# Kernel optimization log

Hardware: AMD Instinct MI355X
Metric: run time of the kernel (lower is better)

Reference implementation:

```python
import jax, jax.numpy as jnp
import numpy as np

N = 5000      # batch entities / prompts
M = 50000     # flattened neighbors
R = 500000    # flattened (neighbor, relation) pairs
D = 768
VOCAB = 10000


def setup_inputs() -> dict:
    key = jax.random.key(0)
    ks = jax.random.split(key, 12)
    start_emb = jax.random.normal(ks[0], (N, D), dtype=jnp.float32)
    prompt_emb = jax.random.normal(ks[1], (N, D), dtype=jnp.float32)
    relation_emb = jax.random.normal(ks[2], (R, D), dtype=jnp.float32)
    neighbor_emb = jax.random.normal(ks[3], (M, D), dtype=jnp.float32)
    count_table = jax.random.normal(ks[4], (VOCAB, D), dtype=jnp.float32) * 0.02
    W = jax.random.normal(ks[5], (1, 4 * D), dtype=jnp.float32) * 0.02
    b = jnp.zeros((1,), dtype=jnp.float32)
    counts = jax.random.randint(ks[6], (R,), 0, VOCAB)
    rel_start_idx = jax.random.randint(ks[7], (R,), 0, N)
    neighbor_idx = jnp.sort(jax.random.randint(ks[8], (R,), 0, M))
    start_idx = jax.random.randint(ks[9], (M,), 0, N)
    return {
        "start_emb": start_emb, "prompt_emb": prompt_emb,
        "relation_emb": relation_emb, "neighbor_emb": neighbor_emb,
        "count_table": count_table, "W": W, "b": b,
        "counts": counts, "rel_start_idx": rel_start_idx,
        "neighbor_idx": neighbor_idx, "start_idx": start_idx,
    }


def _segment_softmax(logits, seg, num_segments):
    # numerically stable softmax within each neighbor segment
    seg_max = jax.ops.segment_max(logits, seg, num_segments=num_segments)
    ex = jnp.exp(logits - seg_max[seg])
    denom = jax.ops.segment_sum(ex, seg, num_segments=num_segments)
    return ex / denom[seg]


def reference(start_emb, prompt_emb, relation_emb, neighbor_emb,
              count_table, W, b,
              counts, rel_start_idx, neighbor_idx, start_idx):
    num_neighbors = neighbor_emb.shape[0]
    # relation_emb = relation_emb * count_embs(counts)   [R, D]
    rel = relation_emb * count_table[counts]
    # per-relation logit: <start_emb[rel_start_idx], rel>  [R]
    s_rel = start_emb[rel_start_idx]
    logits = jnp.sum(s_rel * rel, axis=1)
    # scatter_softmax over neighbor segments, then scatter_add aggregation
    alpha = _segment_softmax(logits, neighbor_idx, num_neighbors)
    rel_agg = jax.ops.segment_sum(rel * alpha[:, None], neighbor_idx,
                                  num_segments=num_neighbors)  # [M, D]
    # gather per-neighbor start / prompt embeddings
    s_n = start_emb[start_idx]      # [M, D]
    p_n = prompt_emb[start_idx]     # [M, D]
    # AttentionScorer: concat then Linear(4D -> 1), squeeze
    combined = jnp.concatenate([s_n, p_n, rel_agg, neighbor_emb], axis=1)
    score = (combined @ W.T + b).squeeze(-1)  # [M]
    return score
```

## Files before the change

### kernel.cpp

```cpp
#include <hip/hip_runtime.h>
#include <math.h>

#define WAVE 64

__device__ inline float wave_reduce_sum(float v) {
    #pragma unroll
    for (int off = 32; off > 0; off >>= 1)
        v += __shfl_xor(v, off, WAVE);
    return v;
}

__device__ inline unsigned int f32_to_e4m3(float a) {
    unsigned int u = __float_as_uint(a);
    unsigned int sgn = (u >> 31) << 7;
    unsigned int absu = u & 0x7FFFFFFFu;
    if (absu < 0x3C800000u) return sgn;
    int exp = (int)(absu >> 23) - 127;
    unsigned int m = absu & 0x7FFFFFu;
    unsigned int keep = m >> 20;
    unsigned int rest = m & 0xFFFFFu;
    if (rest > 0x80000u || (rest == 0x80000u && (keep & 1u))) keep++;
    if (keep == 8u) { keep = 0u; exp += 1; }
    if (exp > 8) { exp = 8; keep = 7u; }
    return sgn | ((unsigned int)(exp + 7) << 3) | keep;
}

__device__ inline float e4m3_to_f32(unsigned int b) {
    unsigned int expm = b & 0x7Fu;
    unsigned int f = ((b & 0x80u) << 24) | ((expm + (120u << 3)) << 20);
    float v = __uint_as_float(f);
    return (expm & 0x78u) ? v : 0.0f;
}

__device__ inline void decode4_fp8(unsigned int u, float& a, float& b, float& c, float& d) {
#if __has_builtin(__builtin_amdgcn_cvt_pk_f32_fp8)
    auto lo = __builtin_amdgcn_cvt_pk_f32_fp8(u, false);
    auto hi = __builtin_amdgcn_cvt_pk_f32_fp8(u, true);
    a = lo[0]; b = lo[1]; c = hi[0]; d = hi[1];
#else
    a = e4m3_to_f32(u & 0xFFu);
    b = e4m3_to_f32((u >> 8) & 0xFFu);
    c = e4m3_to_f32((u >> 16) & 0xFFu);
    d = e4m3_to_f32((u >> 24) & 0xFFu);
#endif
}

__global__ void cvt_fp8_kernel(const float* __restrict__ in,
                               unsigned int* __restrict__ out,
                               int n4, float scale) {
    int i = blockIdx.x * blockDim.x + threadIdx.x;
    if (i >= n4) return;
    float4 v = ((const float4*)in)[i];
    unsigned int b0 = f32_to_e4m3(v.x * scale);
    unsigned int b1 = f32_to_e4m3(v.y * scale);
    unsigned int b2 = f32_to_e4m3(v.z * scale);
    unsigned int b3 = f32_to_e4m3(v.w * scale);
    out[i] = b0 | (b1 << 8) | (b2 << 16) | (b3 << 24);
}

__global__ void entity_dots_kernel(const float* __restrict__ start_emb,
                                   const float* __restrict__ prompt_emb,
                                   const float* __restrict__ W,
                                   float* __restrict__ ew, int N, int D) {
    int wavesPerBlock = blockDim.x >> 6;
    int i = blockIdx.x * wavesPerBlock + (threadIdx.x >> 6);
    int lane = threadIdx.x & 63;
    if (i >= N) return;
    const float* s  = start_emb  + (size_t)i * D;
    const float* p  = prompt_emb + (size_t)i * D;
    const float* w0 = W;
    const float* w1 = W + D;
    float acc = 0.f;
    for (int idx = lane * 4; idx < D; idx += WAVE * 4) {
        float4 sv  = *(const float4*)(s  + idx);
        float4 pv  = *(const float4*)(p  + idx);
        float4 w0v = *(const float4*)(w0 + idx);
        float4 w1v = *(const float4*)(w1 + idx);
        acc = fmaf(sv.x, w0v.x, acc);
        acc = fmaf(sv.y, w0v.y, acc);
        acc = fmaf(sv.z, w0v.z, acc);
        acc = fmaf(sv.w, w0v.w, acc);
        acc = fmaf(pv.x, w1v.x, acc);
        acc = fmaf(pv.y, w1v.y, acc);
        acc = fmaf(pv.z, w1v.z, acc);
        acc = fmaf(pv.w, w1v.w, acc);
    }
    acc = wave_reduce_sum(acc);
    if (lane == 0) ew[i] = acc;
}

__global__ void relation_kernel(const float* __restrict__ relation_emb,
                                const unsigned char* __restrict__ ctf8,
                                const unsigned char* __restrict__ sf8,
                                const float* __restrict__ W,
                                const int* __restrict__ counts,
                                const int* __restrict__ rel_start_idx,
                                float2* __restrict__ lt,
                                int R, int D, float inv_ct_scale) {
    int wavesPerBlock = blockDim.x >> 6;
    int r = blockIdx.x * wavesPerBlock + (threadIdx.x >> 6);
    int lane = threadIdx.x & 63;
    if (r >= R) return;
    const float* re = relation_emb + (size_t)r * D;
    const unsigned int* ct = (const unsigned int*)(ctf8 + (size_t)counts[r] * D);
    const unsigned int* se = (const unsigned int*)(sf8 + (size_t)rel_start_idx[r] * D);
    const float* w2 = W + 2 * (size_t)D;
    float lg = 0.f, tt = 0.f;
    for (int idx = lane * 4; idx < D; idx += WAVE * 4) {
        float4 rv = *(const float4*)(re + idx);
        float4 wv = *(const float4*)(w2 + idx);
        unsigned int cu = ct[idx >> 2];
        unsigned int su = se[idx >> 2];
        float c0, c1, c2, c3, s0, s1, s2, s3;
        decode4_fp8(cu, c0, c1, c2, c3);
        decode4_fp8(su, s0, s1, s2, s3);
        float relx = rv.x * c0;
        float rely = rv.y * c1;
        float relz = rv.z * c2;
        float relw = rv.w * c3;
        lg = fmaf(s0, relx, lg);
        lg = fmaf(s1, rely, lg);
        lg = fmaf(s2, relz, lg);
        lg = fmaf(s3, relw, lg);
        tt = fmaf(wv.x, relx, tt);
        tt = fmaf(wv.y, rely, tt);
        tt = fmaf(wv.z, relz, tt);
        tt = fmaf(wv.w, relw, tt);
    }
    lg = wave_reduce_sum(lg) * inv_ct_scale;
    tt = wave_reduce_sum(tt) * inv_ct_scale;
    if (lane == 0) lt[r] = make_float2(lg, tt);
}

__global__ void segment_kernel(const float2* __restrict__ lt,
                               const int* __restrict__ neighbor_idx,
                               float* __restrict__ c,
                               int M, int R) {
    int m = blockIdx.x * blockDim.x + threadIdx.x;
    if (m >= M) return;
    int lo = 0, hi = R;
    while (lo < hi) {
        int mid = (lo + hi) >> 1;
        if (neighbor_idx[mid] < m) lo = mid + 1; else hi = mid;
    }
    int s = lo;
    hi = R;
    while (lo < hi) {
        int mid = (lo + hi) >> 1;
        if (neighbor_idx[mid] < m + 1) lo = mid + 1; else hi = mid;
    }
    int e = lo;
    if (e <= s) { c[m] = 0.f; return; }
    float mx = -INFINITY;
    for (int i = s; i < e; ++i) mx = fmaxf(mx, lt[i].x);
    float den = 0.f, num = 0.f;
    for (int i = s; i < e; ++i) {
        float2 v = lt[i];
        float ex = expf(v.x - mx);
        den += ex;
        num = fmaf(ex, v.y, num);
    }
    c[m] = num / den;
}

__global__ void score_kernel(const float* __restrict__ neighbor_emb,
                             const float* __restrict__ W,
                             const float* __restrict__ bptr,
                             const int* __restrict__ start_idx,
                             const float* __restrict__ ew,
                             const float* __restrict__ c,
                             float* __restrict__ out,
                             int M, int D) {
    int wavesPerBlock = blockDim.x >> 6;
    int m = blockIdx.x * wavesPerBlock + (threadIdx.x >> 6);
    int lane = threadIdx.x & 63;
    if (m >= M) return;
    const float* nb = neighbor_emb + (size_t)m * D;
    const float* w3 = W + 3 * (size_t)D;
    float acc = 0.f;
    for (int idx = lane * 4; idx < D; idx += WAVE * 4) {
        float4 nv = *(const float4*)(nb + idx);
        float4 wv = *(const float4*)(w3 + idx);
        acc = fmaf(nv.x, wv.x, acc);
        acc = fmaf(nv.y, wv.y, acc);
        acc = fmaf(nv.z, wv.z, acc);
        acc = fmaf(nv.w, wv.w, acc);
    }
    acc = wave_reduce_sum(acc);
    if (lane == 0) {
        out[m] = acc + ew[start_idx[m]] + c[m] + bptr[0];
    }
}

extern "C" void kernel_launch(void* const* d_in, const int* in_sizes, int n_in,
                              void* d_out, int out_size, void* d_ws, size_t ws_size,
                              hipStream_t stream) {
    const float* start_emb    = (const float*)d_in[0];
    const float* prompt_emb   = (const float*)d_in[1];
    const float* relation_emb = (const float*)d_in[2];
    const float* neighbor_emb = (const float*)d_in[3];
    const float* count_table  = (const float*)d_in[4];
    const float* W            = (const float*)d_in[5];
    const float* b            = (const float*)d_in[6];
    const int*   counts        = (const int*)d_in[7];
    const int*   rel_start_idx = (const int*)d_in[8];
    const int*   neighbor_idx  = (const int*)d_in[9];
    const int*   start_idx     = (const int*)d_in[10];

    int D = in_sizes[5] / 4;
    int N = in_sizes[0] / D;
    int R = in_sizes[7];
    int M = in_sizes[10];
    int VOCAB = in_sizes[4] / D;

    const float CT_SCALE = 64.0f;

    char* ws = (char*)d_ws;
    size_t off = 0;
    float*  ew   = (float*)(ws + off);  off += ((size_t)N * 4 + 255) & ~(size_t)255;
    float2* lt   = (float2*)(ws + off); off += ((size_t)R * 8 + 255) & ~(size_t)255;
    float*  c    = (float*)(ws + off);  off += ((size_t)M * 4 + 255) & ~(size_t)255;
    unsigned char* ctf8 = (unsigned char*)(ws + off); off += ((size_t)VOCAB * D + 255) & ~(size_t)255;
    unsigned char* sf8  = (unsigned char*)(ws + off); off += ((size_t)N * D + 255) & ~(size_t)255;
    float*  out  = (float*)d_out;

    {
        int n4 = (VOCAB * D) / 4;
        cvt_fp8_kernel<<<(n4 + 255) / 256, 256, 0, stream>>>(count_table,
                                                             (unsigned int*)ctf8, n4, CT_SCALE);
        int m4 = (N * D) / 4;
        cvt_fp8_kernel<<<(m4 + 255) / 256, 256, 0, stream>>>(start_emb,
                                                             (unsigned int*)sf8, m4, 1.0f);
    }
    {
        int grid = (N + 3) / 4;
        entity_dots_kernel<<<grid, 256, 0, stream>>>(start_emb, prompt_emb, W, ew, N, D);
    }
    {
        int grid = (R + 3) / 4;
        relation_kernel<<<grid, 256, 0, stream>>>(relation_emb, ctf8, sf8, W,
                                                  counts, rel_start_idx, lt, R, D,
                                                  1.0f / CT_SCALE);
    }
    {
        int grid = (M + 255) / 256;
        segment_kernel<<<grid, 256, 0, stream>>>(lt, neighbor_idx, c, M, R);
    }
    {
        int grid = (M + 3) / 4;
        score_kernel<<<grid, 256, 0, stream>>>(neighbor_emb, W, b, start_idx, ew, c, out, M, D);
    }
}
```

Measured before the change: 375.4 us.

## Fuse prologue kernels, merge segment softmax into score, persist relation waves

Merges the two fp8 conversion kernels and the entity-dot kernel into one prologue launch. The segment softmax moves into the score kernel and is now computed cooperatively by a wave instead of a single thread, which removes one launch and the intermediate c buffer. The relation and score kernels get D=768 specialised variants that use a persistent grid, keep W slices in registers, prefetch the next indices, and use nontemporal loads for streamed rows. In exchange, every wave in the score kernel now runs the two binary searches redundantly, and the fixed 2048-block grid may not fill the device optimally.

```diff
diff --git a/kernel.cpp b/kernel.cpp
--- a/kernel.cpp
+++ b/kernel.cpp
@@ -2,11 +2,19 @@
 #include <math.h>
 
 #define WAVE 64
+
+typedef float f32x4 __attribute__((ext_vector_type(4)));
 
 __device__ inline float wave_reduce_sum(float v) {
     #pragma unroll
     for (int off = 32; off > 0; off >>= 1)
         v += __shfl_xor(v, off, WAVE);
+    return v;
+}
+__device__ inline float wave_reduce_max(float v) {
+    #pragma unroll
+    for (int off = 32; off > 0; off >>= 1)
+        v = fmaxf(v, __shfl_xor(v, off, WAVE));
     return v;
 }
 
@@ -45,25 +53,49 @@
 #endif
 }
 
-__global__ void cvt_fp8_kernel(const float* __restrict__ in,
-                               unsigned int* __restrict__ out,
-                               int n4, float scale) {
-    int i = blockIdx.x * blockDim.x + threadIdx.x;
-    if (i >= n4) return;
-    float4 v = ((const float4*)in)[i];
-    unsigned int b0 = f32_to_e4m3(v.x * scale);
-    unsigned int b1 = f32_to_e4m3(v.y * scale);
-    unsigned int b2 = f32_to_e4m3(v.z * scale);
-    unsigned int b3 = f32_to_e4m3(v.w * scale);
-    out[i] = b0 | (b1 << 8) | (b2 << 16) | (b3 << 24);
-}
-
-__global__ void entity_dots_kernel(const float* __restrict__ start_emb,
-                                   const float* __restrict__ prompt_emb,
-                                   const float* __restrict__ W,
-                                   float* __restrict__ ew, int N, int D) {
-    int wavesPerBlock = blockDim.x >> 6;
-    int i = blockIdx.x * wavesPerBlock + (threadIdx.x >> 6);
+__device__ inline unsigned int pack4_fp8(float4 v, float scale) {
+    return f32_to_e4m3(v.x * scale) | (f32_to_e4m3(v.y * scale) << 8) |
+           (f32_to_e4m3(v.z * scale) << 16) | (f32_to_e4m3(v.w * scale) << 24);
+}
+
+__global__ __launch_bounds__(256) void prologue_kernel(
+        const float* __restrict__ count_table,
+        const float* __restrict__ start_emb,
+        const float* __restrict__ prompt_emb,
+        const float* __restrict__ W,
+        unsigned int* __restrict__ ctf8,
+        unsigned int* __restrict__ sf8,
+        float* __restrict__ ew,
+        int ctN16, int sN16, int B_ct, int B_s,
+        int N, int D, float ct_scale) {
+    int b = blockIdx.x;
+    if (b < B_ct) {
+        int i = b * 256 + threadIdx.x;
+        if (i < ctN16) {
+            const float4* in = (const float4*)count_table + (size_t)i * 4;
+            uint4 o;
+            o.x = pack4_fp8(in[0], ct_scale);
+            o.y = pack4_fp8(in[1], ct_scale);
+            o.z = pack4_fp8(in[2], ct_scale);
+            o.w = pack4_fp8(in[3], ct_scale);
+            ((uint4*)ctf8)[i] = o;
+        }
+        return;
+    }
+    if (b < B_ct + B_s) {
+        int i = (b - B_ct) * 256 + threadIdx.x;
+        if (i < sN16) {
+            const float4* in = (const float4*)start_emb + (size_t)i * 4;
+            uint4 o;
+            o.x = pack4_fp8(in[0], 1.0f);
+            o.y = pack4_fp8(in[1], 1.0f);
+            o.z = pack4_fp8(in[2], 1.0f);
+            o.w = pack4_fp8(in[3], 1.0f);
+            ((uint4*)sf8)[i] = o;
+        }
+        return;
+    }
+    int i = (b - B_ct - B_s) * 4 + (threadIdx.x >> 6);
     int lane = threadIdx.x & 63;
     if (i >= N) return;
     const float* s  = start_emb  + (size_t)i * D;
@@ -89,16 +121,147 @@
     if (lane == 0) ew[i] = acc;
 }
 
-__global__ void relation_kernel(const float* __restrict__ relation_emb,
-                                const unsigned char* __restrict__ ctf8,
-                                const unsigned char* __restrict__ sf8,
-                                const float* __restrict__ W,
-                                const int* __restrict__ counts,
-                                const int* __restrict__ rel_start_idx,
-                                float2* __restrict__ lt,
-                                int R, int D, float inv_ct_scale) {
-    int wavesPerBlock = blockDim.x >> 6;
-    int r = blockIdx.x * wavesPerBlock + (threadIdx.x >> 6);
+__global__ __launch_bounds__(256) void relation_kernel768(
+        const float* __restrict__ relation_emb,
+        const unsigned char* __restrict__ ctf8,
+        const unsigned char* __restrict__ sf8,
+        const float* __restrict__ W,
+        const int* __restrict__ counts,
+        const int* __restrict__ rel_start_idx,
+        float2* __restrict__ lt,
+        int R, float inv_ct_scale) {
+    const int D = 768;
+    int lane = threadIdx.x & 63;
+    int gwave = (blockIdx.x * blockDim.x + threadIdx.x) >> 6;
+    int nwaves = (gridDim.x * blockDim.x) >> 6;
+    if (gwave >= R) return;
+
+    const float* w2 = W + 2 * D;
+    float4 wv0 = *(const float4*)(w2 + lane * 4);
+    float4 wv1 = *(const float4*)(w2 + lane * 4 + 256);
+    float4 wv2 = *(const float4*)(w2 + lane * 4 + 512);
+
+    int r = gwave;
+    int cnt = counts[r], st = rel_start_idx[r];
+    while (r < R) {
+        int rn = r + nwaves;
+        int cnt_cur = cnt, st_cur = st;
+        if (rn < R) { cnt = counts[rn]; st = rel_start_idx[rn]; }
+
+        const float* re = relation_emb + (size_t)r * D;
+        const unsigned int* ct = (const unsigned int*)(ctf8 + (size_t)cnt_cur * D);
+        const unsigned int* se = (const unsigned int*)(sf8 + (size_t)st_cur * D);
+
+        f32x4 a0 = __builtin_nontemporal_load((const f32x4*)(re + lane * 4));
+        f32x4 a1 = __builtin_nontemporal_load((const f32x4*)(re + lane * 4 + 256));
+        f32x4 a2 = __builtin_nontemporal_load((const f32x4*)(re + lane * 4 + 512));
+        unsigned int cu0 = ct[lane], cu1 = ct[lane + 64], cu2 = ct[lane + 128];
+        unsigned int su0 = se[lane], su1 = se[lane + 64], su2 = se[lane + 128];
+
+        float lg = 0.f, tt = 0.f;
+        {
+            float c0,c1,c2,c3, s0,s1,s2,s3;
+            decode4_fp8(cu0, c0,c1,c2,c3);
+            decode4_fp8(su0, s0,s1,s2,s3);
+            float x0 = a0.x*c0, x1 = a0.y*c1, x2 = a0.z*c2, x3 = a0.w*c3;
+            lg = fmaf(s0,x0, fmaf(s1,x1, fmaf(s2,x2, fmaf(s3,x3, lg))));
+            tt = fmaf(wv0.x,x0, fmaf(wv0.y,x1, fmaf(wv0.z,x2, fmaf(wv0.w,x3, tt))));
+        }
+        {
+            float c0,c1,c2,c3, s0,s1,s2,s3;
+            decode4_fp8(cu1, c0,c1,c2,c3);
+            decode4_fp8(su1, s0,s1,s2,s3);
+            float x0 = a1.x*c0, x1 = a1.y*c1, x2 = a1.z*c2, x3 = a1.w*c3;
+            lg = fmaf(s0,x0, fmaf(s1,x1, fmaf(s2,x2, fmaf(s3,x3, lg))));
+            tt = fmaf(wv1.x,x0, fmaf(wv1.y,x1, fmaf(wv1.z,x2, fmaf(wv1.w,x3, tt))));
+        }
+        {
+            float c0,c1,c2,c3, s0,s1,s2,s3;
+            decode4_fp8(cu2, c0,c1,c2,c3);
+            decode4_fp8(su2, s0,s1,s2,s3);
+            float x0 = a2.x*c0, x1 = a2.y*c1, x2 = a2.z*c2, x3 = a2.w*c3;
+            lg = fmaf(s0,x0, fmaf(s1,x1, fmaf(s2,x2, fmaf(s3,x3, lg))));
+            tt = fmaf(wv2.x,x0, fmaf(wv2.y,x1, fmaf(wv2.z,x2, fmaf(wv2.w,x3, tt))));
+        }
+        lg = wave_reduce_sum(lg) * inv_ct_scale;
+        tt = wave_reduce_sum(tt) * inv_ct_scale;
+        if (lane == 0) lt[r] = make_float2(lg, tt);
+        r = rn;
+    }
+}
+
+__global__ __launch_bounds__(256) void score_kernel768(
+        const float* __restrict__ neighbor_emb,
+        const float* __restrict__ W,
+        const float* __restrict__ bptr,
+        const int* __restrict__ start_idx,
+        const float* __restrict__ ew,
+        const float2* __restrict__ lt,
+        const int* __restrict__ neighbor_idx,
+        float* __restrict__ out,
+        int M, int R) {
+    const int D = 768;
+    int lane = threadIdx.x & 63;
+    int gwave = (blockIdx.x * blockDim.x + threadIdx.x) >> 6;
+    int nwaves = (gridDim.x * blockDim.x) >> 6;
+    const float* w3 = W + 3 * D;
+    float4 wv0 = *(const float4*)(w3 + lane * 4);
+    float4 wv1 = *(const float4*)(w3 + lane * 4 + 256);
+    float4 wv2 = *(const float4*)(w3 + lane * 4 + 512);
+    float bb = bptr[0];
+
+    for (int m = gwave; m < M; m += nwaves) {
+        int lo = 0, hi = R;
+        while (lo < hi) { int mid = (lo + hi) >> 1; if (neighbor_idx[mid] < m) lo = mid + 1; else hi = mid; }
+        int s = lo;
+        hi = R;
+        while (lo < hi) { int mid = (lo + hi) >> 1; if (neighbor_idx[mid] < m + 1) lo = mid + 1; else hi = mid; }
+        int e = lo;
+
+        const float* nb = neighbor_emb + (size_t)m * D;
+        f32x4 a0 = __builtin_nontemporal_load((const f32x4*)(nb + lane * 4));
+        f32x4 a1 = __builtin_nontemporal_load((const f32x4*)(nb + lane * 4 + 256));
+        f32x4 a2 = __builtin_nontemporal_load((const f32x4*)(nb + lane * 4 + 512));
+
+        float cval = 0.f;
+        if (e > s) {
+            float mx = -INFINITY;
+            for (int i = s + lane; i < e; i += WAVE) mx = fmaxf(mx, lt[i].x);
+            mx = wave_reduce_max(mx);
+            float den = 0.f, num = 0.f;
+            for (int i = s + lane; i < e; i += WAVE) {
+                float2 v = lt[i];
+                float exv = expf(v.x - mx);
+                den += exv;
+                num = fmaf(exv, v.y, num);
+            }
+            den = wave_reduce_sum(den);
+            num = wave_reduce_sum(num);
+            cval = num / den;
+        }
+
+        float acc = 0.f;
+        acc = fmaf(a0.x, wv0.x, acc); acc = fmaf(a0.y, wv0.y, acc);
+        acc = fmaf(a0.z, wv0.z, acc); acc = fmaf(a0.w, wv0.w, acc);
+        acc = fmaf(a1.x, wv1.x, acc); acc = fmaf(a1.y, wv1.y, acc);
+        acc = fmaf(a1.z, wv1.z, acc); acc = fmaf(a1.w, wv1.w, acc);
+        acc = fmaf(a2.x, wv2.x, acc); acc = fmaf(a2.y, wv2.y, acc);
+        acc = fmaf(a2.z, wv2.z, acc); acc = fmaf(a2.w, wv2.w, acc);
+        acc = wave_reduce_sum(acc);
+
+        if (lane == 0) out[m] = acc + ew[start_idx[m]] + cval + bb;
+    }
+}
+
+__global__ void relation_kernel_gen(const float* __restrict__ relation_emb,
+                                    const unsigned char* __restrict__ ctf8,
+                                    const unsigned char* __restrict__ sf8,
+                                    const float* __restrict__ W,
+                                    const int* __restrict__ counts,
+                                    const int* __restrict__ rel_start_idx,
+                                    float2* __restrict__ lt,
+                                    int R, int D, float inv_ct_scale) {
+    int r = blockIdx.x * (blockDim.x >> 6) + (threadIdx.x >> 6);
     int lane = threadIdx.x & 63;
     if (r >= R) return;
     const float* re = relation_emb + (size_t)r * D;
@@ -109,72 +272,52 @@
     for (int idx = lane * 4; idx < D; idx += WAVE * 4) {
         float4 rv = *(const float4*)(re + idx);
         float4 wv = *(const float4*)(w2 + idx);
-        unsigned int cu = ct[idx >> 2];
-        unsigned int su = se[idx >> 2];
-        float c0, c1, c2, c3, s0, s1, s2, s3;
-        decode4_fp8(cu, c0, c1, c2, c3);
-        decode4_fp8(su, s0, s1, s2, s3);
-        float relx = rv.x * c0;
-        float rely = rv.y * c1;
-        float relz = rv.z * c2;
-        float relw = rv.w * c3;
-        lg = fmaf(s0, relx, lg);
-        lg = fmaf(s1, rely, lg);
-        lg = fmaf(s2, relz, lg);
-        lg = fmaf(s3, relw, lg);
-        tt = fmaf(wv.x, relx, tt);
-        tt = fmaf(wv.y, rely, tt);
-        tt = fmaf(wv.z, relz, tt);
-        tt = fmaf(wv.w, relw, tt);
+        float c0,c1,c2,c3, s0,s1,s2,s3;
+        decode4_fp8(ct[idx >> 2], c0,c1,c2,c3);
+        decode4_fp8(se[idx >> 2], s0,s1,s2,s3);
+        float x0 = rv.x*c0, x1 = rv.y*c1, x2 = rv.z*c2, x3 = rv.w*c3;
+        lg = fmaf(s0,x0, fmaf(s1,x1, fmaf(s2,x2, fmaf(s3,x3, lg))));
+        tt = fmaf(wv.x,x0, fmaf(wv.y,x1, fmaf(wv.z,x2, fmaf(wv.w,x3, tt))));
     }
     lg = wave_reduce_sum(lg) * inv_ct_scale;
     tt = wave_reduce_sum(tt) * inv_ct_scale;
     if (lane == 0) lt[r] = make_float2(lg, tt);
 }
 
-__global__ void segment_kernel(const float2* __restrict__ lt,
-                               const int* __restrict__ neighbor_idx,
-                               float* __restrict__ c,
-                               int M, int R) {
-    int m = blockIdx.x * blockDim.x + threadIdx.x;
+__global__ void score_kernel_gen(const float* __restrict__ neighbor_emb,
+                                 const float* __restrict__ W,
+                                 const float* __restrict__ bptr,
+                                 const int* __restrict__ start_idx,
+                                 const float* __restrict__ ew,
+                                 const float2* __restrict__ lt,
+                                 const int* __restrict__ neighbor_idx,
+                                 float* __restrict__ out,
+                                 int M, int R, int D) {
+    int m = blockIdx.x * (blockDim.x >> 6) + (threadIdx.x >> 6);
+    int lane = threadIdx.x & 63;
     if (m >= M) return;
     int lo = 0, hi = R;
-    while (lo < hi) {
-        int mid = (lo + hi) >> 1;
-        if (neighbor_idx[mid] < m) lo = mid + 1; else hi = mid;
-    }
+    while (lo < hi) { int mid = (lo + hi) >> 1; if (neighbor_idx[mid] < m) lo = mid + 1; else hi = mid; }
     int s = lo;
     hi = R;
-    while (lo < hi) {
-        int mid = (lo + hi) >> 1;
-        if (neighbor_idx[mid] < m + 1) lo = mid + 1; else hi = mid;
-    }
+    while (lo < hi) { int mid = (lo + hi) >> 1; if (neighbor_idx[mid] < m + 1) lo = mid + 1; else hi = mid; }
     int e = lo;
-    if (e <= s) { c[m] = 0.f; return; }
-    float mx = -INFINITY;
-    for (int i = s; i < e; ++i) mx = fmaxf(mx, lt[i].x);
-    float den = 0.f, num = 0.f;
-    for (int i = s; i < e; ++i) {
-        float2 v = lt[i];
-        float ex = expf(v.x - mx);
-        den += ex;
-        num = fmaf(ex, v.y, num);
-    }
-    c[m] = num / den;
-}
-
-__global__ void score_kernel(const float* __restrict__ neighbor_emb,
-                             const float* __restrict__ W,
-                             const float* __restrict__ bptr,
-                             const int* __restrict__ start_idx,
-                             const float* __restrict__ ew,
-                             const float* __restrict__ c,
-                             float* __restrict__ out,
-                             int M, int D) {
-    int wavesPerBlock = blockDim.x >> 6;
-    int m = blockIdx.x * wavesPerBlock + (threadIdx.x >> 6);
-    int lane = threadIdx.x & 63;
-    if (m >= M) return;
+    float cval = 0.f;
+    if (e > s) {
+        float mx = -INFINITY;
+        for (int i = s + lane; i < e; i += WAVE) mx = fmaxf(mx, lt[i].x);
+        mx = wave_reduce_max(mx);
+        float den = 0.f, num = 0.f;
+        for (int i = s + lane; i < e; i += WAVE) {
+            float2 v = lt[i];
+            float exv = expf(v.x - mx);
+            den += exv;
+            num = fmaf(exv, v.y, num);
+        }
+        den = wave_reduce_sum(den);
+        num = wave_reduce_sum(num);
+        cval = num / den;
+    }
     const float* nb = neighbor_emb + (size_t)m * D;
     const float* w3 = W + 3 * (size_t)D;
     float acc = 0.f;
@@ -187,9 +330,7 @@
         acc = fmaf(nv.w, wv.w, acc);
     }
     acc = wave_reduce_sum(acc);
-    if (lane == 0) {
-        out[m] = acc + ew[start_idx[m]] + c[m] + bptr[0];
-    }
+    if (lane == 0) out[m] = acc + ew[start_idx[m]] + cval + bptr[0];
 }
 
 extern "C" void kernel_launch(void* const* d_in, const int* in_sizes, int n_in,
@@ -219,35 +360,34 @@
     size_t off = 0;
     float*  ew   = (float*)(ws + off);  off += ((size_t)N * 4 + 255) & ~(size_t)255;
     float2* lt   = (float2*)(ws + off); off += ((size_t)R * 8 + 255) & ~(size_t)255;
-    float*  c    = (float*)(ws + off);  off += ((size_t)M * 4 + 255) & ~(size_t)255;
     unsigned char* ctf8 = (unsigned char*)(ws + off); off += ((size_t)VOCAB * D + 255) & ~(size_t)255;
     unsigned char* sf8  = (unsigned char*)(ws + off); off += ((size_t)N * D + 255) & ~(size_t)255;
     float*  out  = (float*)d_out;
 
-    {
-        int n4 = (VOCAB * D) / 4;
-        cvt_fp8_kernel<<<(n4 + 255) / 256, 256, 0, stream>>>(count_table,
-                                                             (unsigned int*)ctf8, n4, CT_SCALE);
-        int m4 = (N * D) / 4;
-        cvt_fp8_kernel<<<(m4 + 255) / 256, 256, 0, stream>>>(start_emb,
-                                                             (unsigned int*)sf8, m4, 1.0f);
-    }
-    {
-        int grid = (N + 3) / 4;
-        entity_dots_kernel<<<grid, 256, 0, stream>>>(start_emb, prompt_emb, W, ew, N, D);
-    }
-    {
-        int grid = (R + 3) / 4;
-        relation_kernel<<<grid, 256, 0, stream>>>(relation_emb, ctf8, sf8, W,
-                                                  counts, rel_start_idx, lt, R, D,
-                                                  1.0f / CT_SCALE);
-    }
-    {
-        int grid = (M + 255) / 256;
-        segment_kernel<<<grid, 256, 0, stream>>>(lt, neighbor_idx, c, M, R);
-    }
-    {
-        int grid = (M + 3) / 4;
-        score_kernel<<<grid, 256, 0, stream>>>(neighbor_emb, W, b, start_idx, ew, c, out, M, D);
-    }
-}
+    int ctN16 = (VOCAB * D) / 16;
+    int sN16  = (N * D) / 16;
+    int B_ct  = (ctN16 + 255) / 256;
+    int B_s   = (sN16 + 255) / 256;
+    int B_k1  = (N + 3) / 4;
+    prologue_kernel<<<B_ct + B_s + B_k1, 256, 0, stream>>>(
+        count_table, start_emb, prompt_emb, W,
+        (unsigned int*)ctf8, (unsigned int*)sf8, ew,
+        ctN16, sN16, B_ct, B_s, N, D, CT_SCALE);
+
+    if (D == 768) {
+        int blocks2 = 2048;
+        if (blocks2 > (R + 3) / 4) blocks2 = (R + 3) / 4;
+        relation_kernel768<<<blocks2, 256, 0, stream>>>(
+            relation_emb, ctf8, sf8, W, counts, rel_start_idx, lt, R, 1.0f / CT_SCALE);
+
+        int blocks4 = 2048;
+        if (blocks4 > (M + 3) / 4) blocks4 = (M + 3) / 4;
+        score_kernel768<<<blocks4, 256, 0, stream>>>(
+            neighbor_emb, W, b, start_idx, ew, lt, neighbor_idx, out, M, R);
+    } else {
+        relation_kernel_gen<<<(R + 3) / 4, 256, 0, stream>>>(
+            relation_emb, ctf8, sf8, W, counts, rel_start_idx, lt, R, D, 1.0f / CT_SCALE);
+        score_kernel_gen<<<(M + 3) / 4, 256, 0, stream>>>(
+            neighbor_emb, W, b, start_idx, ew, lt, neighbor_idx, out, M, R, D);
+    }
+}
```

Measured after the change: 422.7 us. 1.13x slower.
